# Performance work log

Hardware: AMD Instinct MI355X
Metric: run time of the kernel (lower is better)

## Reference

```python
import jax, jax.numpy as jnp
import numpy as np

W_PAD = 1  # reflection pad / stencil half-width
CLAMP_MIN = 0.071
EPS = 1e-05


def _laplacian_kernel():
    k = 2 * W_PAD + 1
    ker = -jnp.ones((1, 1, k, k, k), dtype=jnp.float32)
    ker = ker.at[0, 0, W_PAD, W_PAD, W_PAD].set(float(k * k * k - 1))
    return ker  # [O=1, I=1, 3, 3, 3]


def _boundary_weight(pred):
    # pred: [B, L, D, H, W] raw logits
    B, L, D, H, Wd = pred.shape
    ps = jax.nn.softmax(pred, axis=1).astype(jnp.float32)
    # reflect-pad spatial dims by 1, then clamp (matches torch: pad then clamp)
    p = jnp.pad(ps, ((0, 0), (0, 0), (1, 1), (1, 1), (1, 1)), mode='reflect')
    p = jnp.clip(p, CLAMP_MIN)
    # single-channel 3x3x3 stencil applied independently per (batch, label)
    x = p.reshape(B * L, 1, D + 2, H + 2, Wd + 2)
    bt = jax.lax.conv_general_dilated(
        x, _laplacian_kernel(), window_strides=(1, 1, 1), padding='VALID',
        dimension_numbers=('NCDHW', 'OIDHW', 'NCDHW'))
    bt = jnp.abs(bt).reshape(B, L, D, H, Wd)
    bt = jax.lax.stop_gradient(bt)  # torch .detach()
    return 0.5 / (bt + 0.5)


def _dice_bpm(y_pred, y_true, bpm):
    vol_axes = tuple(range(2, y_pred.ndim))  # spatial dims
    top = 2.0 * jnp.sum(y_true * y_pred * bpm, axis=vol_axes)
    bottom = jnp.clip(jnp.sum((y_true + y_pred) * bpm, axis=vol_axes), EPS)
    return -jnp.mean(top / bottom)


def setup_inputs() -> dict:
    key = jax.random.key(0)
    k1, k2 = jax.random.split(key)
    shape = (2, 8, 128, 128, 128)
    pred = jax.random.normal(k1, shape, dtype=jnp.float32)
    target = jax.random.uniform(k2, shape, dtype=jnp.float32)
    return {"pred": pred, "target": target}


def reference(pred, target):
    focal_weight = _boundary_weight(pred)
    return _dice_bpm(pred, target, focal_weight)
```

## Files before the change

kernel.cpp:

```cpp
#include <hip/hip_runtime.h>

constexpr int Dd = 128, Hh = 128, Ww = 128;
constexpr int B_ = 2, L_ = 8;
constexpr int HW = Hh * Ww;
constexpr int S_SP = Dd * HW;
constexpr float CLAMP_MIN = 0.071f;
constexpr float EPS = 1e-5f;

constexpr int HC = 8;
constexpr int NHC = Hh / HC;
constexpr int DPB = 4;
constexpr int NDQ = Dd / DPB;
constexpr int NBLK = B_ * NHC * NDQ;

__global__ __launch_bounds__(256, 2) void fused_kernel(
    const float* __restrict__ pred, const float* __restrict__ tgt,
    float* __restrict__ partial) {
  const int blk = blockIdx.x;
  const int b   = blk >> 9;
  const int rem = blk & 511;
  const int hc  = rem >> 5;
  const int dq  = rem & 31;
  const int tid = threadIdx.x;
  const int wl  = tid & 63;
  const int hl  = tid >> 6;
  const int d   = dq * DPB + hl;
  const int h0  = hc * HC;
  const int w0  = wl * 2;
  const int dm = (d == 0) ? 1 : d - 1;
  const int dp = (d == Dd - 1) ? Dd - 2 : d + 1;
  const float* Pb = pred + (size_t)b * L_ * S_SP;
  const float* Tb = tgt  + (size_t)b * L_ * S_SP + (size_t)d * HW;
  const float* plane[3] = {Pb + (size_t)dm * HW,
                           Pb + (size_t)d  * HW,
                           Pb + (size_t)dp * HW};

  float ps2[L_][2], s2c[L_][2], cprev[L_][2], rawprev[L_][2];
  float top[L_], bot[L_];
#pragma unroll
  for (int l = 0; l < L_; ++l) {
    top[l] = 0.f; bot[l] = 0.f;
    ps2[l][0] = ps2[l][1] = 0.f;
    s2c[l][0] = s2c[l][1] = 0.f;
    cprev[l][0] = cprev[l][1] = 0.f;
    rawprev[l][0] = rawprev[l][1] = 0.f;
  }

  for (int k = 0; k < HC + 2; ++k) {
    const int r  = h0 - 1 + k;
    const int rr = (r < 0) ? 1 : ((r > Hh - 1) ? Hh - 2 : r);
    const int roff = rr * Ww + w0;

    float2 tv[L_];
    if (k >= 2) {
      const size_t tbase = (size_t)(r - 1) * Ww + w0;
#pragma unroll
      for (int l = 0; l < L_; ++l)
        tv[l] = *(const float2*)(Tb + (size_t)l * S_SP + tbase);
    }

    float2 v[3][L_];
#pragma unroll
    for (int pl = 0; pl < 3; ++pl)
#pragma unroll
      for (int l = 0; l < L_; ++l)
        v[pl][l] = *(const float2*)(plane[pl] + (size_t)l * S_SP + roff);

    float s3d[L_][2];
    float ctr[L_][2], rawc[L_][2];
#pragma unroll
    for (int l = 0; l < L_; ++l) s3d[l][0] = s3d[l][1] = 0.f;
#pragma unroll
    for (int pl = 0; pl < 3; ++pl) {
      float p0[L_], p1[L_];
      float s0 = 0.f, s1 = 0.f;
#pragma unroll
      for (int l = 0; l < L_; ++l) {
        p0[l] = __expf(v[pl][l].x); s0 += p0[l];
        p1[l] = __expf(v[pl][l].y); s1 += p1[l];
      }
      const float i0 = 1.f / s0, i1 = 1.f / s1;
#pragma unroll
      for (int l = 0; l < L_; ++l) {
        p0[l] = fmaxf(p0[l] * i0, CLAMP_MIN);
        p1[l] = fmaxf(p1[l] * i1, CLAMP_MIN);
      }
#pragma unroll
      for (int l = 0; l < L_; ++l) {
        float lf = __shfl_up(p1[l], 1, 64);
        if (wl == 0) lf = p1[l];
        float rf = __shfl_down(p0[l], 1, 64);
        if (wl == 63) rf = p0[l];
        s3d[l][0] += lf + p0[l] + p1[l];
        s3d[l][1] += p0[l] + p1[l] + rf;
        if (pl == 1) {
          ctr[l][0] = p0[l]; ctr[l][1] = p1[l];
          rawc[l][0] = v[pl][l].x; rawc[l][1] = v[pl][l].y;
        }
      }
    }

    if (k >= 2) {
#pragma unroll
      for (int l = 0; l < L_; ++l) {
        {
          float bt = fabsf(27.f * cprev[l][0] - (ps2[l][0] + s3d[l][0]));
          float bw = 0.5f / (bt + 0.5f);
          top[l] += tv[l].x * rawprev[l][0] * bw;
          bot[l] += (tv[l].x + rawprev[l][0]) * bw;
        }
        {
          float bt = fabsf(27.f * cprev[l][1] - (ps2[l][1] + s3d[l][1]));
          float bw = 0.5f / (bt + 0.5f);
          top[l] += tv[l].y * rawprev[l][1] * bw;
          bot[l] += (tv[l].y + rawprev[l][1]) * bw;
        }
      }
    }

#pragma unroll
    for (int l = 0; l < L_; ++l) {
      ps2[l][0] = s2c[l][0] + s3d[l][0]; ps2[l][1] = s2c[l][1] + s3d[l][1];
      s2c[l][0] = s3d[l][0];             s2c[l][1] = s3d[l][1];
      cprev[l][0] = ctr[l][0];           cprev[l][1] = ctr[l][1];
      rawprev[l][0] = rawc[l][0];        rawprev[l][1] = rawc[l][1];
    }
  }

#pragma unroll
  for (int l = 0; l < L_; ++l) {
#pragma unroll
    for (int o = 32; o > 0; o >>= 1) {
      top[l] += __shfl_down(top[l], o, 64);
      bot[l] += __shfl_down(bot[l], o, 64);
    }
  }
  __shared__ float red[4][16];
  if (wl == 0) {
#pragma unroll
    for (int l = 0; l < L_; ++l) {
      red[hl][2 * l]     = top[l];
      red[hl][2 * l + 1] = bot[l];
    }
  }
  __syncthreads();
  if (tid < 16) {
    float s = red[0][tid] + red[1][tid] + red[2][tid] + red[3][tid];
    partial[blk * 16 + tid] = s;
  }
}

__global__ void finalize_kernel(const float* __restrict__ partial, float* __restrict__ out) {
  __shared__ float rr[16];
  const int t = threadIdx.x;
  const int p = t >> 4;
  const int k = t & 15;
  const int b = p >> 3;
  const int l = p & 7;
  float top = 0.f, bot = 0.f;
  for (int m = 0; m < 32; ++m) {
    int blk = b * 512 + k * 32 + m;
    top += partial[blk * 16 + 2 * l];
    bot += partial[blk * 16 + 2 * l + 1];
  }
#pragma unroll
  for (int o = 8; o > 0; o >>= 1) {
    top += __shfl_down(top, o, 16);
    bot += __shfl_down(bot, o, 16);
  }
  if (k == 0) rr[p] = 2.f * top / fmaxf(bot, EPS);
  __syncthreads();
  if (t == 0) {
    float s = 0.f;
#pragma unroll
    for (int i = 0; i < 16; ++i) s += rr[i];
    out[0] = -s / 16.f;
  }
}

extern "C" void kernel_launch(void* const* d_in, const int* in_sizes, int n_in,
                              void* d_out, int out_size, void* d_ws, size_t ws_size,
                              hipStream_t stream) {
  const float* pred = (const float*)d_in[0];
  const float* tgt  = (const float*)d_in[1];
  float* partial = (float*)d_ws;
  fused_kernel<<<NBLK, 256, 0, stream>>>(pred, tgt, partial);
  finalize_kernel<<<1, 256, 0, stream>>>(partial, (float*)d_out);
}
```

Before: 314.6 us.

## Software-pipeline row loads with double-buffered registers and scalarize depth index

Restructures the row loop into a double-buffered software pipeline: the logits for the next row are loaded into a second register set while the current row is computed, so global-load latency overlaps the exp/softmax work. The depth index is forced into a scalar register with readfirstlane so the plane base addresses can be computed uniformly. The center plane is processed last so its clamped probabilities stay available without separate copies. The cost is a much larger register footprint (two 3x8 float2 buffers), which could spill or cut occupancy under the 256x2 launch bound.

Result: slower. 479.2 us (+52.3%).

```diff
diff --git a/kernel.cpp b/kernel.cpp
--- a/kernel.cpp
+++ b/kernel.cpp
@@ -24,18 +24,18 @@
   const int tid = threadIdx.x;
   const int wl  = tid & 63;
   const int hl  = tid >> 6;
-  const int d   = dq * DPB + hl;
+  const int d   = __builtin_amdgcn_readfirstlane(dq * DPB + hl);
   const int h0  = hc * HC;
   const int w0  = wl * 2;
   const int dm = (d == 0) ? 1 : d - 1;
   const int dp = (d == Dd - 1) ? Dd - 2 : d + 1;
   const float* Pb = pred + (size_t)b * L_ * S_SP;
   const float* Tb = tgt  + (size_t)b * L_ * S_SP + (size_t)d * HW;
-  const float* plane[3] = {Pb + (size_t)dm * HW,
-                           Pb + (size_t)d  * HW,
-                           Pb + (size_t)dp * HW};
-
-  float ps2[L_][2], s2c[L_][2], cprev[L_][2], rawprev[L_][2];
+  const float* P0 = Pb + (size_t)dm * HW;
+  const float* P1 = Pb + (size_t)d  * HW;
+  const float* P2 = Pb + (size_t)dp * HW;
+
+  float ps2[L_][2], s2c[L_][2], cprev[L_][2];
   float top[L_], bot[L_];
 #pragma unroll
   for (int l = 0; l < L_; ++l) {
@@ -43,88 +43,110 @@
     ps2[l][0] = ps2[l][1] = 0.f;
     s2c[l][0] = s2c[l][1] = 0.f;
     cprev[l][0] = cprev[l][1] = 0.f;
-    rawprev[l][0] = rawprev[l][1] = 0.f;
-  }
-
-  for (int k = 0; k < HC + 2; ++k) {
-    const int r  = h0 - 1 + k;
-    const int rr = (r < 0) ? 1 : ((r > Hh - 1) ? Hh - 2 : r);
-    const int roff = rr * Ww + w0;
-
-    float2 tv[L_];
-    if (k >= 2) {
-      const size_t tbase = (size_t)(r - 1) * Ww + w0;
-#pragma unroll
-      for (int l = 0; l < L_; ++l)
-        tv[l] = *(const float2*)(Tb + (size_t)l * S_SP + tbase);
-    }
-
-    float2 v[3][L_];
-#pragma unroll
-    for (int pl = 0; pl < 3; ++pl)
-#pragma unroll
-      for (int l = 0; l < L_; ++l)
-        v[pl][l] = *(const float2*)(plane[pl] + (size_t)l * S_SP + roff);
-
-    float s3d[L_][2];
-    float ctr[L_][2], rawc[L_][2];
-#pragma unroll
-    for (int l = 0; l < L_; ++l) s3d[l][0] = s3d[l][1] = 0.f;
-#pragma unroll
-    for (int pl = 0; pl < 3; ++pl) {
-      float p0[L_], p1[L_];
+  }
+
+  float2 vA[3][L_], vB[3][L_];
+  float s3d[L_][2];
+  float pc0[L_], pc1[L_];
+  float rawp[L_][2];
+  float2 tv[L_];
+
+  auto rowOff = [&](int r) -> int {
+    int rr = (r < 0) ? 1 : ((r > Hh - 1) ? Hh - 2 : r);
+    return rr * Ww + w0;
+  };
+  auto LOADP = [&](int r, float2 (&v)[3][L_]) {
+    const int ro = rowOff(r);
+#pragma unroll
+    for (int l = 0; l < L_; ++l) v[0][l] = *(const float2*)(P0 + (size_t)l * S_SP + ro);
+#pragma unroll
+    for (int l = 0; l < L_; ++l) v[1][l] = *(const float2*)(P1 + (size_t)l * S_SP + ro);
+#pragma unroll
+    for (int l = 0; l < L_; ++l) v[2][l] = *(const float2*)(P2 + (size_t)l * S_SP + ro);
+  };
+  auto LOADT = [&](int o) {
+    const int ro = o * Ww + w0;
+#pragma unroll
+    for (int l = 0; l < L_; ++l) tv[l] = *(const float2*)(Tb + (size_t)l * S_SP + ro);
+  };
+  auto COPYRAW = [&](const float2 (&v)[3][L_]) {
+#pragma unroll
+    for (int l = 0; l < L_; ++l) { rawp[l][0] = v[1][l].x; rawp[l][1] = v[1][l].y; }
+  };
+  auto COMPUTE = [&](const float2 (&v)[3][L_]) {
+#pragma unroll
+    for (int l = 0; l < L_; ++l) { s3d[l][0] = 0.f; s3d[l][1] = 0.f; }
+    const int order[3] = {0, 2, 1};
+#pragma unroll
+    for (int oi = 0; oi < 3; ++oi) {
+      const int pl = order[oi];
+      float e0[L_], e1[L_];
       float s0 = 0.f, s1 = 0.f;
 #pragma unroll
       for (int l = 0; l < L_; ++l) {
-        p0[l] = __expf(v[pl][l].x); s0 += p0[l];
-        p1[l] = __expf(v[pl][l].y); s1 += p1[l];
+        e0[l] = __expf(v[pl][l].x); s0 += e0[l];
+        e1[l] = __expf(v[pl][l].y); s1 += e1[l];
       }
       const float i0 = 1.f / s0, i1 = 1.f / s1;
 #pragma unroll
       for (int l = 0; l < L_; ++l) {
-        p0[l] = fmaxf(p0[l] * i0, CLAMP_MIN);
-        p1[l] = fmaxf(p1[l] * i1, CLAMP_MIN);
-      }
-#pragma unroll
-      for (int l = 0; l < L_; ++l) {
-        float lf = __shfl_up(p1[l], 1, 64);
-        if (wl == 0) lf = p1[l];
-        float rf = __shfl_down(p0[l], 1, 64);
-        if (wl == 63) rf = p0[l];
-        s3d[l][0] += lf + p0[l] + p1[l];
-        s3d[l][1] += p0[l] + p1[l] + rf;
-        if (pl == 1) {
-          ctr[l][0] = p0[l]; ctr[l][1] = p1[l];
-          rawc[l][0] = v[pl][l].x; rawc[l][1] = v[pl][l].y;
-        }
-      }
-    }
-
-    if (k >= 2) {
-#pragma unroll
-      for (int l = 0; l < L_; ++l) {
-        {
-          float bt = fabsf(27.f * cprev[l][0] - (ps2[l][0] + s3d[l][0]));
-          float bw = 0.5f / (bt + 0.5f);
-          top[l] += tv[l].x * rawprev[l][0] * bw;
-          bot[l] += (tv[l].x + rawprev[l][0]) * bw;
-        }
-        {
-          float bt = fabsf(27.f * cprev[l][1] - (ps2[l][1] + s3d[l][1]));
-          float bw = 0.5f / (bt + 0.5f);
-          top[l] += tv[l].y * rawprev[l][1] * bw;
-          bot[l] += (tv[l].y + rawprev[l][1]) * bw;
-        }
-      }
-    }
-
+        float a = fmaxf(e0[l] * i0, CLAMP_MIN);
+        float c = fmaxf(e1[l] * i1, CLAMP_MIN);
+        float lf = __shfl_up(c, 1, 64);
+        if (wl == 0) lf = c;
+        float rf = __shfl_down(a, 1, 64);
+        if (wl == 63) rf = a;
+        s3d[l][0] += lf + a + c;
+        s3d[l][1] += a + c + rf;
+        pc0[l] = a; pc1[l] = c;
+      }
+    }
+  };
+  auto EMIT = [&]() {
+#pragma unroll
+    for (int l = 0; l < L_; ++l) {
+      {
+        float bt = fabsf(27.f * cprev[l][0] - (ps2[l][0] + s3d[l][0]));
+        float bw = 0.5f / (bt + 0.5f);
+        top[l] += tv[l].x * rawp[l][0] * bw;
+        bot[l] += (tv[l].x + rawp[l][0]) * bw;
+      }
+      {
+        float bt = fabsf(27.f * cprev[l][1] - (ps2[l][1] + s3d[l][1]));
+        float bw = 0.5f / (bt + 0.5f);
+        top[l] += tv[l].y * rawp[l][1] * bw;
+        bot[l] += (tv[l].y + rawp[l][1]) * bw;
+      }
+    }
+  };
+  auto ROTATE = [&]() {
 #pragma unroll
     for (int l = 0; l < L_; ++l) {
       ps2[l][0] = s2c[l][0] + s3d[l][0]; ps2[l][1] = s2c[l][1] + s3d[l][1];
       s2c[l][0] = s3d[l][0];             s2c[l][1] = s3d[l][1];
-      cprev[l][0] = ctr[l][0];           cprev[l][1] = ctr[l][1];
-      rawprev[l][0] = rawc[l][0];        rawprev[l][1] = rawc[l][1];
-    }
+      cprev[l][0] = pc0[l];              cprev[l][1] = pc1[l];
+    }
+  };
+
+  LOADP(h0 - 1, vA);
+  LOADP(h0,     vB);
+  COMPUTE(vA); ROTATE();
+  LOADP(h0 + 1, vA);
+  COMPUTE(vB); ROTATE();
+
+  for (int kk = 2; kk < 10; kk += 2) {
+    COPYRAW(vB);
+    LOADT(h0 + kk - 2);
+    LOADP(h0 + kk, vB);
+    COMPUTE(vA);
+    EMIT();
+    ROTATE();
+    COPYRAW(vA);
+    LOADT(h0 + kk - 1);
+    if (kk < 8) LOADP(h0 + kk + 1, vA);
+    COMPUTE(vB);
+    EMIT();
+    ROTATE();
   }
 
 #pragma unroll
```

## Split labels across wavefronts and compute softmax denominators through LDS

Applied to the files above, without the earlier changes.

Each of the eight wavefronts in a 512-thread block now owns one label, instead of every thread holding all eight labels in registers. The softmax denominator is formed by a cross-wave sum over the labels in shared memory, and each block covers one depth slice and a 16-row strip. Block IDs are remapped so that neighbouring depth planes are scheduled together for cache reuse. This is meant to cut register pressure and raise occupancy, at the cost of two block barriers per row and extra LDS traffic.

Measured after the change: 325.1 us. 1.03x slower.

```diff
diff --git a/kernel.cpp b/kernel.cpp
--- a/kernel.cpp
+++ b/kernel.cpp
@@ -7,146 +7,109 @@
 constexpr float CLAMP_MIN = 0.071f;
 constexpr float EPS = 1e-5f;
 
-constexpr int HC = 8;
+constexpr int HC = 16;
 constexpr int NHC = Hh / HC;
-constexpr int DPB = 4;
-constexpr int NDQ = Dd / DPB;
-constexpr int NBLK = B_ * NHC * NDQ;
+constexpr int NBLK = B_ * Dd * NHC;
 
-__global__ __launch_bounds__(256, 2) void fused_kernel(
+__global__ __launch_bounds__(512, 3) void fused_kernel(
     const float* __restrict__ pred, const float* __restrict__ tgt,
     float* __restrict__ partial) {
-  const int blk = blockIdx.x;
-  const int b   = blk >> 9;
-  const int rem = blk & 511;
-  const int hc  = rem >> 5;
-  const int dq  = rem & 31;
+  const int bid = blockIdx.x;
+  const int blk = (bid & 7) * 256 + (bid >> 3);
+  const int d  = blk & 127;
+  const int hc = (blk >> 7) & 7;
+  const int b  = blk >> 10;
   const int tid = threadIdx.x;
   const int wl  = tid & 63;
-  const int hl  = tid >> 6;
-  const int d   = dq * DPB + hl;
+  const int lab = __builtin_amdgcn_readfirstlane(tid >> 6);
+  const int w0  = wl * 2;
   const int h0  = hc * HC;
-  const int w0  = wl * 2;
   const int dm = (d == 0) ? 1 : d - 1;
   const int dp = (d == Dd - 1) ? Dd - 2 : d + 1;
-  const float* Pb = pred + (size_t)b * L_ * S_SP;
-  const float* Tb = tgt  + (size_t)b * L_ * S_SP + (size_t)d * HW;
-  const float* plane[3] = {Pb + (size_t)dm * HW,
-                           Pb + (size_t)d  * HW,
-                           Pb + (size_t)dp * HW};
+  const float* PL = pred + ((size_t)b * L_ + lab) * S_SP;
+  const float* TL = tgt  + ((size_t)b * L_ + lab) * S_SP + (size_t)d * HW;
+  const float* P0 = PL + (size_t)dm * HW;
+  const float* P1 = PL + (size_t)d  * HW;
+  const float* P2 = PL + (size_t)dp * HW;
 
-  float ps2[L_][2], s2c[L_][2], cprev[L_][2], rawprev[L_][2];
-  float top[L_], bot[L_];
-#pragma unroll
-  for (int l = 0; l < L_; ++l) {
-    top[l] = 0.f; bot[l] = 0.f;
-    ps2[l][0] = ps2[l][1] = 0.f;
-    s2c[l][0] = s2c[l][1] = 0.f;
-    cprev[l][0] = cprev[l][1] = 0.f;
-    rawprev[l][0] = rawprev[l][1] = 0.f;
-  }
+  __shared__ float eSh[3][L_][Ww + 1];
+  __shared__ float iSh[3][Ww];
+
+  float ps2[2] = {0.f, 0.f}, s2c[2] = {0.f, 0.f};
+  float cprev[2] = {0.f, 0.f}, rawprev[2] = {0.f, 0.f};
+  float top = 0.f, bot = 0.f;
 
   for (int k = 0; k < HC + 2; ++k) {
     const int r  = h0 - 1 + k;
     const int rr = (r < 0) ? 1 : ((r > Hh - 1) ? Hh - 2 : r);
-    const int roff = rr * Ww + w0;
+    const int ro = rr * Ww + w0;
 
-    float2 tv[L_];
+    const float2 v0 = *(const float2*)(P0 + ro);
+    const float2 v1 = *(const float2*)(P1 + ro);
+    const float2 v2 = *(const float2*)(P2 + ro);
+    float2 tv = make_float2(0.f, 0.f);
+    if (k >= 2) tv = *(const float2*)(TL + (r - 1) * Ww + w0);
+
+    const float e0x = __expf(v0.x), e0y = __expf(v0.y);
+    const float e1x = __expf(v1.x), e1y = __expf(v1.y);
+    const float e2x = __expf(v2.x), e2y = __expf(v2.y);
+
+    *(float2*)&eSh[0][lab][w0] = make_float2(e0x, e0y);
+    *(float2*)&eSh[1][lab][w0] = make_float2(e1x, e1y);
+    *(float2*)&eSh[2][lab][w0] = make_float2(e2x, e2y);
+    __syncthreads();
+    if (tid < 3 * Ww) {
+      const int pl = tid >> 7, w = tid & 127;
+      float s = eSh[pl][0][w] + eSh[pl][1][w] + eSh[pl][2][w] + eSh[pl][3][w]
+              + eSh[pl][4][w] + eSh[pl][5][w] + eSh[pl][6][w] + eSh[pl][7][w];
+      iSh[pl][w] = 1.f / s;
+    }
+    __syncthreads();
+    const float2 i0 = *(const float2*)&iSh[0][w0];
+    const float2 i1 = *(const float2*)&iSh[1][w0];
+    const float2 i2 = *(const float2*)&iSh[2][w0];
+
+    const float cx = fmaxf(e1x * i1.x, CLAMP_MIN);
+    const float cy = fmaxf(e1y * i1.y, CLAMP_MIN);
+    float qx = fmaxf(e0x * i0.x, CLAMP_MIN) + cx + fmaxf(e2x * i2.x, CLAMP_MIN);
+    float qy = fmaxf(e0y * i0.y, CLAMP_MIN) + cy + fmaxf(e2y * i2.y, CLAMP_MIN);
+
+    float lf = __shfl_up(qy, 1, 64);
+    if (wl == 0) lf = qy;
+    float rf = __shfl_down(qx, 1, 64);
+    if (wl == 63) rf = qx;
+    const float h3x = lf + qx + qy;
+    const float h3y = qx + qy + rf;
+
     if (k >= 2) {
-      const size_t tbase = (size_t)(r - 1) * Ww + w0;
-#pragma unroll
-      for (int l = 0; l < L_; ++l)
-        tv[l] = *(const float2*)(Tb + (size_t)l * S_SP + tbase);
-    }
-
-    float2 v[3][L_];
-#pragma unroll
-    for (int pl = 0; pl < 3; ++pl)
-#pragma unroll
-      for (int l = 0; l < L_; ++l)
-        v[pl][l] = *(const float2*)(plane[pl] + (size_t)l * S_SP + roff);
-
-    float s3d[L_][2];
-    float ctr[L_][2], rawc[L_][2];
-#pragma unroll
-    for (int l = 0; l < L_; ++l) s3d[l][0] = s3d[l][1] = 0.f;
-#pragma unroll
-    for (int pl = 0; pl < 3; ++pl) {
-      float p0[L_], p1[L_];
-      float s0 = 0.f, s1 = 0.f;
-#pragma unroll
-      for (int l = 0; l < L_; ++l) {
-        p0[l] = __expf(v[pl][l].x); s0 += p0[l];
-        p1[l] = __expf(v[pl][l].y); s1 += p1[l];
+      {
+        float bt = fabsf(27.f * cprev[0] - (ps2[0] + h3x));
+        float bw = 0.5f / (bt + 0.5f);
+        top += tv.x * rawprev[0] * bw;
+        bot += (tv.x + rawprev[0]) * bw;
       }
-      const float i0 = 1.f / s0, i1 = 1.f / s1;
-#pragma unroll
-      for (int l = 0; l < L_; ++l) {
-        p0[l] = fmaxf(p0[l] * i0, CLAMP_MIN);
-        p1[l] = fmaxf(p1[l] * i1, CLAMP_MIN);
-      }
-#pragma unroll
-      for (int l = 0; l < L_; ++l) {
-        float lf = __shfl_up(p1[l], 1, 64);
-        if (wl == 0) lf = p1[l];
-        float rf = __shfl_down(p0[l], 1, 64);
-        if (wl == 63) rf = p0[l];
-        s3d[l][0] += lf + p0[l] + p1[l];
-        s3d[l][1] += p0[l] + p1[l] + rf;
-        if (pl == 1) {
-          ctr[l][0] = p0[l]; ctr[l][1] = p1[l];
-          rawc[l][0] = v[pl][l].x; rawc[l][1] = v[pl][l].y;
-        }
+      {
+        float bt = fabsf(27.f * cprev[1] - (ps2[1] + h3y));
+        float bw = 0.5f / (bt + 0.5f);
+        top += tv.y * rawprev[1] * bw;
+        bot += (tv.y + rawprev[1]) * bw;
       }
     }
 
-    if (k >= 2) {
-#pragma unroll
-      for (int l = 0; l < L_; ++l) {
-        {
-          float bt = fabsf(27.f * cprev[l][0] - (ps2[l][0] + s3d[l][0]));
-          float bw = 0.5f / (bt + 0.5f);
-          top[l] += tv[l].x * rawprev[l][0] * bw;
-          bot[l] += (tv[l].x + rawprev[l][0]) * bw;
-        }
-        {
-          float bt = fabsf(27.f * cprev[l][1] - (ps2[l][1] + s3d[l][1]));
-          float bw = 0.5f / (bt + 0.5f);
-          top[l] += tv[l].y * rawprev[l][1] * bw;
-          bot[l] += (tv[l].y + rawprev[l][1]) * bw;
-        }
-      }
-    }
-
-#pragma unroll
-    for (int l = 0; l < L_; ++l) {
-      ps2[l][0] = s2c[l][0] + s3d[l][0]; ps2[l][1] = s2c[l][1] + s3d[l][1];
-      s2c[l][0] = s3d[l][0];             s2c[l][1] = s3d[l][1];
-      cprev[l][0] = ctr[l][0];           cprev[l][1] = ctr[l][1];
-      rawprev[l][0] = rawc[l][0];        rawprev[l][1] = rawc[l][1];
-    }
+    ps2[0] = s2c[0] + h3x; ps2[1] = s2c[1] + h3y;
+    s2c[0] = h3x;          s2c[1] = h3y;
+    cprev[0] = cx;         cprev[1] = cy;
+    rawprev[0] = v1.x;     rawprev[1] = v1.y;
   }
 
 #pragma unroll
-  for (int l = 0; l < L_; ++l) {
-#pragma unroll
-    for (int o = 32; o > 0; o >>= 1) {
-      top[l] += __shfl_down(top[l], o, 64);
-      bot[l] += __shfl_down(bot[l], o, 64);
-    }
+  for (int o = 32; o > 0; o >>= 1) {
+    top += __shfl_down(top, o, 64);
+    bot += __shfl_down(bot, o, 64);
   }
-  __shared__ float red[4][16];
   if (wl == 0) {
-#pragma unroll
-    for (int l = 0; l < L_; ++l) {
-      red[hl][2 * l]     = top[l];
-      red[hl][2 * l + 1] = bot[l];
-    }
-  }
-  __syncthreads();
-  if (tid < 16) {
-    float s = red[0][tid] + red[1][tid] + red[2][tid] + red[3][tid];
-    partial[blk * 16 + tid] = s;
+    partial[blk * 16 + 2 * lab]     = top;
+    partial[blk * 16 + 2 * lab + 1] = bot;
   }
 }
 
@@ -158,8 +121,8 @@
   const int b = p >> 3;
   const int l = p & 7;
   float top = 0.f, bot = 0.f;
-  for (int m = 0; m < 32; ++m) {
-    int blk = b * 512 + k * 32 + m;
+  for (int m = 0; m < 64; ++m) {
+    int blk = b * 1024 + k * 64 + m;
     top += partial[blk * 16 + 2 * l];
     bot += partial[blk * 16 + 2 * l + 1];
   }
@@ -184,6 +147,6 @@
   const float* pred = (const float*)d_in[0];
   const float* tgt  = (const float*)d_in[1];
   float* partial = (float*)d_ws;
-  fused_kernel<<<NBLK, 256, 0, stream>>>(pred, tgt, partial);
+  fused_kernel<<<NBLK, 512, 0, stream>>>(pred, tgt, partial);
   finalize_kernel<<<1, 256, 0, stream>>>(partial, (float*)d_out);
 }
```
